# Kernel tuning notes

Measured on AMD Instinct MI355X. Metric: run time of the kernel, lower is better.

Reference implementation:

```python
import jax, jax.numpy as jnp
import numpy as np

D_MODEL = 512
HEAD = 64

def setup_inputs() -> dict:
    key = jax.random.key(0)
    ks = jax.random.split(key, 7)
    s_in = 1.0 / np.sqrt(D_MODEL)
    x = jax.random.normal(ks[0], (4, 4096, D_MODEL), dtype=jnp.float32)
    Wk = jax.random.uniform(ks[1], (D_MODEL, HEAD), jnp.float32, -s_in, s_in)
    bk = jax.random.uniform(ks[2], (HEAD,), jnp.float32, -s_in, s_in)
    Wq = jax.random.uniform(ks[3], (D_MODEL, HEAD), jnp.float32, -s_in, s_in)
    bq = jax.random.uniform(ks[4], (HEAD,), jnp.float32, -s_in, s_in)
    Wv = jax.random.uniform(ks[5], (D_MODEL, HEAD), jnp.float32, -s_in, s_in)
    bv = jax.random.uniform(ks[6], (HEAD,), jnp.float32, -s_in, s_in)
    return {"x": x, "Wk": Wk, "bk": bk, "Wq": Wq, "bq": bq, "Wv": Wv, "bv": bv}

def reference(x, Wk, bk, Wq, bq, Wv, bv):
    B, T, C = x.shape
    k = x @ Wk + bk            # [B,T,H]
    q = x @ Wq + bq            # [B,T,H]
    v = x @ Wv + bv            # [B,T,H]
    scale = C ** (-0.5)
    # NOTE: original computes k @ q^T (keys index rows), softmax over query axis
    w = jnp.einsum('bkh,bqh->bkq', k, q) * scale  # [B,T,T]
    w = jax.nn.softmax(w, axis=-1)
    out = jnp.einsum('bkq,bqh->bkh', w, v)        # [B,T,H]
    return out
```

## Files before the change

kernel.cpp:

```cpp
#include <hip/hip_runtime.h>


#define DM 512
#define HD 64
#define TSEQ 4096
#define KSCALE (1.4426950408889634f * 0.04419417382415922f)

typedef __attribute__((ext_vector_type(8))) __bf16 bf16x8;
typedef __attribute__((ext_vector_type(4))) __bf16 bf16x4;
typedef __attribute__((ext_vector_type(2))) __bf16 bf16x2;
typedef __attribute__((ext_vector_type(4))) float f32x4;
typedef __attribute__((ext_vector_type(16))) float f32x16;
typedef __attribute__((ext_vector_type(4))) unsigned int uint4v;

__device__ __forceinline__ float fast_exp2(float x) {
#if __has_builtin(__builtin_amdgcn_exp2f)
    return __builtin_amdgcn_exp2f(x);
#else
    return exp2f(x);
#endif
}

__device__ __forceinline__ bf16x8 ld_bf16x8(const unsigned short* p) {
    return __builtin_bit_cast(bf16x8, *(const uint4v*)p);
}
__device__ __forceinline__ f32x4 mfma16(bf16x8 a, bf16x8 b, f32x4 c) {
    return __builtin_amdgcn_mfma_f32_16x16x32_bf16(a, b, c, 0, 0, 0);
}
__device__ __forceinline__ f32x16 mfma32(bf16x8 a, bf16x8 b, f32x16 c) {
    return __builtin_amdgcn_mfma_f32_32x32x16_bf16(a, b, c, 0, 0, 0);
}

typedef const __attribute__((address_space(1))) unsigned int* gas_t;
typedef __attribute__((address_space(3))) unsigned int* las_t;
__device__ __forceinline__ void async_cp16(const void* g, void* l) {
    __builtin_amdgcn_global_load_lds((gas_t)(unsigned long long)g,
                                     (las_t)(unsigned int)(unsigned long long)l,
                                     16, 0, 0);
}

__global__ __launch_bounds__(256) void prep_wt(const float* __restrict__ Wk,
                                               const float* __restrict__ Wq,
                                               const float* __restrict__ Wv,
                                               unsigned short* __restrict__ WT) {
    int e = blockIdx.x * 256 + threadIdx.x;
    int m = e >> 15;
    int idx = e & 32767;
    int h = idx >> 9;
    int cc = idx & 511;
    const float* W = (m == 0) ? Wk : ((m == 1) ? Wq : Wv);
    float v = W[cc * HD + h];
    if (m == 0) v *= KSCALE;
    ((__bf16*)WT)[m * 32768 + h * DM + cc] = (__bf16)v;
}

__global__ __launch_bounds__(512, 4) void proj(const float* __restrict__ x,
                                               const unsigned short* __restrict__ WT,
                                               const float* __restrict__ bk,
                                               const float* __restrict__ bq,
                                               const float* __restrict__ bv,
                                               unsigned short* __restrict__ Kw,
                                               unsigned short* __restrict__ Qw,
                                               unsigned short* __restrict__ VTw) {
    __shared__ alignas(16) float xs[16384];
    const int tid = threadIdx.x;
    const int wv = tid >> 6, lane = tid & 63;
    const int c = lane & 15, quad = lane >> 4;
    const int ng = wv & 3, rg = wv >> 2;
    const int bx = blockIdx.x;
    const int n0 = ng * 16;

#pragma unroll
    for (int r = 0; r < 8; ++r) {
        int cid = r * 512 + tid;
        int row = cid >> 7, pos = cid & 127;
        int g = (pos & ~7) | ((pos ^ row) & 7);
        async_cp16((const char*)x + (size_t)(bx * 32 + row) * 2048 + g * 16,
                   (char*)xs + r * 8192 + wv * 1024);
    }
    __builtin_amdgcn_s_waitcnt(0x0f70);
    __syncthreads();

    const int arow = rg * 16 + c;
    const unsigned short* wtb = WT + (n0 + c) * DM + quad * 8;
    f32x4 acc[3];
#pragma unroll
    for (int m = 0; m < 3; ++m) acc[m] = (f32x4){0.f, 0.f, 0.f, 0.f};

#pragma unroll
    for (int ks = 0; ks < 16; ++ks) {
        int p0 = ks * 8 + quad * 2;
        int sp0 = (p0 & ~7) | ((p0 ^ arow) & 7);
        int sp1 = ((p0 + 1) & ~7) | (((p0 + 1) ^ arow) & 7);
        f32x4 xa = *(const f32x4*)((const char*)xs + arow * 2048 + sp0 * 16);
        f32x4 xb = *(const f32x4*)((const char*)xs + arow * 2048 + sp1 * 16);
        bf16x8 af;
        af[0] = (__bf16)xa[0]; af[1] = (__bf16)xa[1]; af[2] = (__bf16)xa[2]; af[3] = (__bf16)xa[3];
        af[4] = (__bf16)xb[0]; af[5] = (__bf16)xb[1]; af[6] = (__bf16)xb[2]; af[7] = (__bf16)xb[3];
#pragma unroll
        for (int m = 0; m < 3; ++m) {
            bf16x8 bf = ld_bf16x8(wtb + m * 32768 + ks * 32);
            acc[m] = mfma16(af, bf, acc[m]);
        }
    }

    const int row0 = bx * 32 + rg * 16 + quad * 4;
#pragma unroll
    for (int m = 0; m < 3; ++m) {
        const float* bp = (m == 0) ? bk : ((m == 1) ? bq : bv);
        float bias = bp[n0 + c];
        if (m == 0) bias *= KSCALE;
        if (m < 2) {
            __bf16* dst = (__bf16*)((m == 0) ? Kw : Qw);
#pragma unroll
            for (int r = 0; r < 4; ++r)
                dst[(row0 + r) * HD + n0 + c] = (__bf16)(acc[m][r] + bias);
        } else {
            bf16x4 pk;
#pragma unroll
            for (int r = 0; r < 4; ++r) pk[r] = (__bf16)(acc[m][r] + bias);
            int b = bx >> 7;
            int rowb = (bx & 127) * 32 + rg * 16 + quad * 4;
            *(bf16x4*)(VTw + ((size_t)(b * 64 + n0 + c)) * TSEQ + rowb) = pk;
        }
    }
}

__global__ __launch_bounds__(512, 2) void attn(const unsigned short* __restrict__ Kw,
                                               const unsigned short* __restrict__ Qw,
                                               const unsigned short* __restrict__ VTw,
                                               float* __restrict__ Op,
                                               float* __restrict__ Lp) {
    __shared__ alignas(16) char smem[131072];

    const int tid = threadIdx.x;
    const int wv = tid >> 6, lane = tid & 63;
    const int l5 = lane >> 5, l31 = lane & 31;
    const int rg = wv >> 2, jc = wv & 3;
    const int bx = blockIdx.x;
    const int lb = (bx & 7) * 32 + (bx >> 3);
    const int batch = lb >> 6, js = (lb >> 5) & 1, tile = lb & 31;
    const int rowbase = batch * TSEQ + tile * 128;

    bf16x8 kf[2][4];
#pragma unroll
    for (int it = 0; it < 2; ++it) {
        const unsigned short* kp = Kw + (size_t)(rowbase + rg * 64 + it * 32 + l31) * HD;
#pragma unroll
        for (int ks = 0; ks < 4; ++ks) kf[it][ks] = ld_bf16x8(kp + ks * 16 + l5 * 8);
    }

    const int jrow = jc * 32 + l31;
    int qoff[4];
#pragma unroll
    for (int ks = 0; ks < 4; ++ks)
        qoff[ks] = jrow * 128 + (((ks * 2 + l5) ^ (jrow & 7)) * 16);
    int voff[2][2];
#pragma unroll
    for (int ht = 0; ht < 2; ++ht)
#pragma unroll
        for (int k2 = 0; k2 < 2; ++k2) {
            int h = ht * 32 + l31;
            voff[ht][k2] = h * 256 + (((jc * 4 + k2 * 2 + l5) ^ (h & 15)) * 16);
        }

    const char* qg = (const char*)(Qw + (size_t)(batch * TSEQ + js * 2048) * HD);
    const char* vg = (const char*)(VTw + (size_t)batch * 64 * TSEQ + js * 2048);
    const int L1 = 512 + tid;
    const int qgo0 = ((tid >> 3) * 128) + (((tid & 7) ^ ((tid >> 3) & 7)) * 16);
    const int qgo1 = ((L1 >> 3) * 128) + (((L1 & 7) ^ ((L1 >> 3) & 7)) * 16);
    const int vgo0 = ((tid >> 4) * 8192) + (((tid & 15) ^ ((tid >> 4) & 15)) * 16);
    const int vgo1 = ((L1 >> 4) * 8192) + (((L1 & 15) ^ ((L1 >> 4) & 15)) * 16);

    f32x16 o00, o01, o10, o11;
#pragma unroll
    for (int r = 0; r < 16; ++r) { o00[r] = 0.f; o01[r] = 0.f; o10[r] = 0.f; o11[r] = 0.f; }
    float lac0 = 0.f, lac1 = 0.f;

    auto STAGE = [&](int t) {
        char* nb = smem + (t & 3) * 32768;
        async_cp16(qg + t * 16384 + qgo0, nb + wv * 1024);
        async_cp16(qg + t * 16384 + qgo1, nb + 8192 + wv * 1024);
        async_cp16(vg + t * 256 + vgo0, nb + 16384 + wv * 1024);
        async_cp16(vg + t * 256 + vgo1, nb + 16384 + 8192 + wv * 1024);
    };

    auto COMPUTE = [&](int jt) {
        const char* cb = smem + (jt & 3) * 32768;
        const unsigned short* QL = (const unsigned short*)cb;
        const unsigned short* VL = (const unsigned short*)(cb + 16384);

        f32x16 s0, s1;
#pragma unroll
        for (int r = 0; r < 16; ++r) { s0[r] = 0.f; s1[r] = 0.f; }
#pragma unroll
        for (int ks = 0; ks < 4; ++ks) {
            bf16x8 qa = ld_bf16x8((const unsigned short*)((const char*)QL + qoff[ks]));
            s0 = mfma32(qa, kf[0][ks], s0);
            s1 = mfma32(qa, kf[1][ks], s1);
        }

        unsigned int pk0[8], pk1[8];
#pragma unroll
        for (int m = 0; m < 8; ++m) {
            float a0 = fast_exp2(s0[2 * m]), a1 = fast_exp2(s0[2 * m + 1]);
            float b0 = fast_exp2(s1[2 * m]), b1 = fast_exp2(s1[2 * m + 1]);
            lac0 += a0 + a1;
            lac1 += b0 + b1;
            bf16x2 ta; ta[0] = (__bf16)a0; ta[1] = (__bf16)a1;
            bf16x2 tb; tb[0] = (__bf16)b0; tb[1] = (__bf16)b1;
            pk0[m] = __builtin_bit_cast(unsigned int, ta);
            pk1[m] = __builtin_bit_cast(unsigned int, tb);
        }

#pragma unroll
        for (int k2 = 0; k2 < 2; ++k2) {
            bf16x8 pb0, pb1;
            {
                unsigned int A0 = pk0[k2 * 4 + 0], A1 = pk0[k2 * 4 + 1];
                unsigned int B0 = pk0[k2 * 4 + 2], B1 = pk0[k2 * 4 + 3];
                unsigned int t0 = l5 ? A0 : B0, t1 = l5 ? A1 : B1;
                unsigned int r0 = (unsigned int)__shfl_xor((int)t0, 32, 64);
                unsigned int r1 = (unsigned int)__shfl_xor((int)t1, 32, 64);
                uint4v u;
                u[0] = l5 ? r0 : A0; u[1] = l5 ? r1 : A1;
                u[2] = l5 ? B0 : r0; u[3] = l5 ? B1 : r1;
                pb0 = __builtin_bit_cast(bf16x8, u);
            }
            {
                unsigned int A0 = pk1[k2 * 4 + 0], A1 = pk1[k2 * 4 + 1];
                unsigned int B0 = pk1[k2 * 4 + 2], B1 = pk1[k2 * 4 + 3];
                unsigned int t0 = l5 ? A0 : B0, t1 = l5 ? A1 : B1;
                unsigned int r0 = (unsigned int)__shfl_xor((int)t0, 32, 64);
                unsigned int r1 = (unsigned int)__shfl_xor((int)t1, 32, 64);
                uint4v u;
                u[0] = l5 ? r0 : A0; u[1] = l5 ? r1 : A1;
                u[2] = l5 ? B0 : r0; u[3] = l5 ? B1 : r1;
                pb1 = __builtin_bit_cast(bf16x8, u);
            }
            bf16x8 vf0 = ld_bf16x8((const unsigned short*)((const char*)VL + voff[0][k2]));
            bf16x8 vf1 = ld_bf16x8((const unsigned short*)((const char*)VL + voff[1][k2]));
            o00 = mfma32(vf0, pb0, o00);
            o01 = mfma32(vf0, pb1, o01);
            o10 = mfma32(vf1, pb0, o10);
            o11 = mfma32(vf1, pb1, o11);
        }
    };

    STAGE(0); STAGE(1); STAGE(2);
    __builtin_amdgcn_sched_barrier(0);
#pragma unroll 1
    for (int jt = 0; jt < 13; ++jt) {
        __builtin_amdgcn_s_waitcnt(0x0f78);
        __builtin_amdgcn_s_barrier();
        __builtin_amdgcn_sched_barrier(0);
        STAGE(jt + 3);
        __builtin_amdgcn_sched_barrier(0);
        COMPUTE(jt);
    }
    __builtin_amdgcn_s_waitcnt(0x0f78);
    __builtin_amdgcn_s_barrier();
    __builtin_amdgcn_sched_barrier(0);
    COMPUTE(13);
    __builtin_amdgcn_s_waitcnt(0x0f74);
    __builtin_amdgcn_s_barrier();
    __builtin_amdgcn_sched_barrier(0);
    COMPUTE(14);
    __builtin_amdgcn_s_waitcnt(0x0f70);
    __builtin_amdgcn_s_barrier();
    __builtin_amdgcn_sched_barrier(0);
    COMPUTE(15);

    lac0 += __shfl_xor(lac0, 32, 64);
    lac1 += __shfl_xor(lac1, 32, 64);
    __syncthreads();
    float* OCp = (float*)smem;
    float* ldsl = (float*)(smem + 34816);
    if (l5 == 0) {
        ldsl[jc * 128 + rg * 64 + l31] = lac0;
        ldsl[jc * 128 + rg * 64 + 32 + l31] = lac1;
    }

#pragma unroll
    for (int ph = 0; ph < 4; ++ph) {
        const int ht = ph >> 1, ih = ph & 1;
        __syncthreads();
        if (rg == ih) {
            const f32x16 oa = ht ? o10 : o00;
            const f32x16 ob = ht ? o11 : o01;
#pragma unroll
            for (int r = 0; r < 16; ++r) {
                int hr = (r & 3) + 8 * (r >> 2) + 4 * l5;
                OCp[(jc * 32 + hr) * 68 + l31] = oa[r];
                OCp[(jc * 32 + hr) * 68 + 32 + l31] = ob[r];
            }
        }
        __syncthreads();
#pragma unroll
        for (int rep = 0; rep < 4; ++rep) {
            int idx = rep * 512 + tid;
            int i = idx >> 5, hr = idx & 31;
            float v = OCp[(0 * 32 + hr) * 68 + i] + OCp[(1 * 32 + hr) * 68 + i]
                    + OCp[(2 * 32 + hr) * 68 + i] + OCp[(3 * 32 + hr) * 68 + i];
            Op[(size_t)js * 1048576 + (size_t)(rowbase + ih * 64 + i) * HD + ht * 32 + hr] = v;
        }
        if (ph == 0 && tid < 128) {
            float L = ldsl[tid] + ldsl[128 + tid] + ldsl[256 + tid] + ldsl[384 + tid];
            Lp[js * 16384 + rowbase + tid] = L;
        }
    }
}

__global__ __launch_bounds__(512) void fin(const float* __restrict__ Op,
                                           const float* __restrict__ Lp,
                                           float* __restrict__ out) {
    int idx = blockIdx.x * 512 + threadIdx.x;
    int e = idx * 4;
    int row = e >> 6;
    f32x4 a = *(const f32x4*)(Op + e);
    f32x4 b = *(const f32x4*)(Op + 1048576 + e);
    float L = Lp[row] + Lp[16384 + row];
    f32x4 r;
#pragma unroll
    for (int k = 0; k < 4; ++k) r[k] = (a[k] + b[k]) / L;
    *(f32x4*)(out + e) = r;
}

extern "C" void kernel_launch(void* const* d_in, const int* in_sizes, int n_in,
                              void* d_out, int out_size, void* d_ws, size_t ws_size,
                              hipStream_t stream) {
    (void)in_sizes; (void)n_in; (void)out_size; (void)ws_size;
    const float* x  = (const float*)d_in[0];
    const float* Wk = (const float*)d_in[1];
    const float* bk = (const float*)d_in[2];
    const float* Wq = (const float*)d_in[3];
    const float* bq = (const float*)d_in[4];
    const float* Wv = (const float*)d_in[5];
    const float* bv = (const float*)d_in[6];

    char* ws = (char*)d_ws;
    unsigned short* WT  = (unsigned short*)(ws);
    unsigned short* Kw  = (unsigned short*)(ws + 196608);
    unsigned short* Qw  = (unsigned short*)(ws + 2293760);
    unsigned short* VTw = (unsigned short*)(ws + 4390912);
    float* Opart        = (float*)(ws + 6488064);
    float* Lpart        = (float*)(ws + 14876672);
    float* outp = (float*)d_out;

    hipLaunchKernelGGL(prep_wt, dim3(384), dim3(256), 0, stream, Wk, Wq, Wv, WT);
    hipLaunchKernelGGL(proj, dim3(512), dim3(512), 0, stream,
                       x, WT, bk, bq, bv, Kw, Qw, VTw);
    hipLaunchKernelGGL(attn, dim3(256), dim3(512), 0, stream, Kw, Qw, VTw, Opart, Lpart);
    hipLaunchKernelGGL(fin, dim3(512), dim3(512), 0, stream, Opart, Lpart, outp);
}
```

Measured before the change: 137.4 us.

## Give each wave a private double-buffered Q/V slice to drop block barriers

Each wave now stages only the 32 Q rows and V columns it consumes into its own 16KB LDS region, using a 2-deep per-wave double buffer instead of a shared 4-deep block-wide ring. This removes the s_barrier in the main loop, so waves only wait on their own async copies. The cost is that waves sharing the same jc now load duplicate data into LDS, and the prefetch depth drops from three tiles to one, which may expose global latency. The LDS swizzle patterns are redone for the narrower per-wave tiles.

Measured after the change: 137.1 us. No clear change (-0.3%).

```diff
diff --git a/kernel.cpp b/kernel.cpp
--- a/kernel.cpp
+++ b/kernel.cpp
@@ -150,27 +150,34 @@
         for (int ks = 0; ks < 4; ++ks) kf[it][ks] = ld_bf16x8(kp + ks * 16 + l5 * 8);
     }
 
-    const int jrow = jc * 32 + l31;
+    char* wbase = smem + wv * 16384;
+
     int qoff[4];
 #pragma unroll
     for (int ks = 0; ks < 4; ++ks)
-        qoff[ks] = jrow * 128 + (((ks * 2 + l5) ^ (jrow & 7)) * 16);
+        qoff[ks] = l31 * 128 + (((ks * 2 + l5) ^ (l31 & 7)) * 16);
     int voff[2][2];
 #pragma unroll
     for (int ht = 0; ht < 2; ++ht)
 #pragma unroll
         for (int k2 = 0; k2 < 2; ++k2) {
             int h = ht * 32 + l31;
-            voff[ht][k2] = h * 256 + (((jc * 4 + k2 * 2 + l5) ^ (h & 15)) * 16);
-        }
-
-    const char* qg = (const char*)(Qw + (size_t)(batch * TSEQ + js * 2048) * HD);
-    const char* vg = (const char*)(VTw + (size_t)batch * 64 * TSEQ + js * 2048);
-    const int L1 = 512 + tid;
-    const int qgo0 = ((tid >> 3) * 128) + (((tid & 7) ^ ((tid >> 3) & 7)) * 16);
-    const int qgo1 = ((L1 >> 3) * 128) + (((L1 & 7) ^ ((L1 >> 3) & 7)) * 16);
-    const int vgo0 = ((tid >> 4) * 8192) + (((tid & 15) ^ ((tid >> 4) & 15)) * 16);
-    const int vgo1 = ((L1 >> 4) * 8192) + (((L1 & 15) ^ ((L1 >> 4) & 15)) * 16);
+            int k = k2 * 2 + l5;
+            voff[ht][k2] = h * 64 + (((k + h) & 3) * 16);
+        }
+
+    const char* qg = (const char*)(Qw + ((size_t)batch * TSEQ + js * 2048 + jc * 32) * HD);
+    const char* vg = (const char*)(VTw + (size_t)batch * 64 * TSEQ) + js * 4096 + jc * 64;
+    int qo[4], vo[4];
+    {
+        const int kk = ((lane & 3) + 4 - ((lane >> 2) & 3)) & 3;
+#pragma unroll
+        for (int op = 0; op < 4; ++op) {
+            int r = (lane >> 3) + 8 * op;
+            qo[op] = r * 128 + (((lane & 7) ^ (lane >> 3)) * 16);
+            vo[op] = ((lane >> 2) + 16 * op) * 8192 + kk * 16;
+        }
+    }
 
     f32x16 o00, o01, o10, o11;
 #pragma unroll
@@ -178,17 +185,19 @@
     float lac0 = 0.f, lac1 = 0.f;
 
     auto STAGE = [&](int t) {
-        char* nb = smem + (t & 3) * 32768;
-        async_cp16(qg + t * 16384 + qgo0, nb + wv * 1024);
-        async_cp16(qg + t * 16384 + qgo1, nb + 8192 + wv * 1024);
-        async_cp16(vg + t * 256 + vgo0, nb + 16384 + wv * 1024);
-        async_cp16(vg + t * 256 + vgo1, nb + 16384 + 8192 + wv * 1024);
+        char* nb = wbase + (t & 1) * 8192;
+#pragma unroll
+        for (int op = 0; op < 4; ++op)
+            async_cp16(qg + t * 16384 + qo[op], nb + op * 1024);
+#pragma unroll
+        for (int op = 0; op < 4; ++op)
+            async_cp16(vg + t * 256 + vo[op], nb + 4096 + op * 1024);
     };
 
     auto COMPUTE = [&](int jt) {
-        const char* cb = smem + (jt & 3) * 32768;
+        const char* cb = wbase + (jt & 1) * 8192;
         const unsigned short* QL = (const unsigned short*)cb;
-        const unsigned short* VL = (const unsigned short*)(cb + 16384);
+        const unsigned short* VL = (const unsigned short*)(cb + 4096);
 
         f32x16 s0, s1;
 #pragma unroll
@@ -247,27 +256,17 @@
         }
     };
 
-    STAGE(0); STAGE(1); STAGE(2);
-    __builtin_amdgcn_sched_barrier(0);
+    __builtin_amdgcn_s_waitcnt(0x0f70);
+    STAGE(0);
 #pragma unroll 1
-    for (int jt = 0; jt < 13; ++jt) {
+    for (int jt = 0; jt < 15; ++jt) {
+        STAGE(jt + 1);
+        __builtin_amdgcn_sched_barrier(0);
         __builtin_amdgcn_s_waitcnt(0x0f78);
-        __builtin_amdgcn_s_barrier();
-        __builtin_amdgcn_sched_barrier(0);
-        STAGE(jt + 3);
         __builtin_amdgcn_sched_barrier(0);
         COMPUTE(jt);
     }
-    __builtin_amdgcn_s_waitcnt(0x0f78);
-    __builtin_amdgcn_s_barrier();
-    __builtin_amdgcn_sched_barrier(0);
-    COMPUTE(13);
-    __builtin_amdgcn_s_waitcnt(0x0f74);
-    __builtin_amdgcn_s_barrier();
-    __builtin_amdgcn_sched_barrier(0);
-    COMPUTE(14);
     __builtin_amdgcn_s_waitcnt(0x0f70);
-    __builtin_amdgcn_s_barrier();
     __builtin_amdgcn_sched_barrier(0);
     COMPUTE(15);
 
```
